# Kernel tuning notes

Measured on AMD Instinct MI355X. Metric: run time of the kernel, lower is better.

## Reference

```python
import jax, jax.numpy as jnp
import numpy as np

WINDOW_SYNC = 20   # min(20, T//2) with T=8192
WINDOW_SURGE = 10
BN_EPS = 1e-5      # BatchNorm1d eval-mode, running_mean=0, running_var=1


def _corr_matrix(x):
    # x: [w, A] observations x variables -> [A, A] Pearson correlation
    xc = x - x.mean(0)
    cov = xc.T @ xc
    d = jnp.sqrt(jnp.diag(cov))
    return cov / (d[:, None] * d[None, :])


def _offdiag_mean(C):
    A = C.shape[0]
    return (C.sum() - jnp.trace(C)) / (A * (A - 1))


def _rolling_offdiag_corr(returns, window):
    # mean off-diagonal correlation over each trailing window [i-window, i)
    T, A = returns.shape
    starts = jnp.arange(T - window)
    def one(s):
        w = jax.lax.dynamic_slice(returns, (s, 0), (window, A))
        return _offdiag_mean(_corr_matrix(w))
    return jax.vmap(one)(starts)


def setup_inputs() -> dict:
    key = jax.random.key(0)
    ks = jax.random.split(key, 10)
    T, A, H = 8192, 128, 128
    returns_sequence = jax.random.normal(ks[0], (T, A), dtype=jnp.float32) * 0.02
    positions = jax.random.normal(ks[1], (A,), dtype=jnp.float32)
    s1 = 1.0 / np.sqrt(2 * A)
    s2 = 1.0 / np.sqrt(H)
    s3 = 1.0 / np.sqrt(H // 2)
    return {
        "returns_sequence": returns_sequence,
        "positions": positions,
        "w1": jax.random.uniform(ks[2], (2 * A, H), jnp.float32, -s1, s1),
        "b1": jax.random.uniform(ks[3], (H,), jnp.float32, -s1, s1),
        "gamma": jnp.ones((H,), jnp.float32),
        "beta": jnp.zeros((H,), jnp.float32),
        "w2": jax.random.uniform(ks[4], (H, H // 2), jnp.float32, -s2, s2),
        "b2": jax.random.uniform(ks[5], (H // 2,), jnp.float32, -s2, s2),
        "w3": jax.random.uniform(ks[6], (H // 2, 3), jnp.float32, -s3, s3),
        "b3": jax.random.uniform(ks[7], (3,), jnp.float32, -s3, s3),
    }


def reference(returns_sequence, positions, w1, b1, gamma, beta, w2, b2, w3, b3):
    returns = returns_sequence
    T, A = returns.shape

    # ---- herding index ----
    cs_std = jnp.std(returns, axis=1, ddof=1)                 # [T]
    herding_trend = -jnp.diff(cs_std).mean()
    avg_dispersion = cs_std.mean()
    herding_index = jnp.clip(herding_trend / (avg_dispersion + 1e-6) + 0.5, 0.0, 1.0)

    # ---- synchronization ----
    corr = _corr_matrix(returns)                              # [A, A]
    avg_correlation = _offdiag_mean(corr)
    rolling = _rolling_offdiag_corr(returns, WINDOW_SYNC)     # [T-20]
    phase_locking = (rolling > 0.7).astype(jnp.float32).mean()
    eigvals = jnp.linalg.eigvalsh(corr)
    sync_indicator = eigvals.max() / A
    sync_risk = jnp.minimum(1.0, sync_indicator * avg_correlation)

    # ---- diversity loss ----
    return_diversity = 1.0 - jnp.abs(corr).mean()             # includes diagonal (as in torch)
    pa = jnp.abs(positions)
    position_diversity = 1.0 - (pa / pa.sum()).max()
    diversity_loss = 1.0 - jnp.sqrt(return_diversity * position_diversity)

    # ---- correlation surge ----
    rolling10 = _rolling_offdiag_corr(returns, WINDOW_SURGE)  # [T-10]
    recent = rolling10[-5:].mean()
    historical = rolling10[:-5].mean()
    surge_raw = jnp.clip((recent - historical) / historical, 0.0, 1.0)
    correlation_surge = jnp.where(historical > 0, surge_raw, 0.0)

    # ---- phase coupling (pairwise sign concordance) ----
    signs = jnp.sign(returns)                                 # [T, A]
    classes = jnp.array([-1.0, 0.0, 1.0], dtype=returns.dtype)
    I = (signs[None, :, :] == classes[:, None, None]).astype(returns.dtype)  # [3, T, A]
    M = jnp.einsum('cta,ctb->ab', I, I) / T                   # eq-fraction matrix [A, A]
    avg_concordance = _offdiag_mean(M)
    phase_coupling = jnp.clip((avg_concordance - 0.5) * 2.0, 0.0, 1.0)

    # ---- herding detector MLP (BatchNorm1d in eval mode) ----
    feats = jnp.concatenate([returns[-1], positions])         # [2A]
    h = jax.nn.relu(feats @ w1 + b1)
    h = gamma * (h / jnp.sqrt(1.0 + BN_EPS)) + beta
    h = jax.nn.relu(h @ w2 + b2)
    logits = h @ w3 + b3
    herding_severity = jax.nn.softmax(logits)[2]

    collective_risk = (herding_index + sync_risk + diversity_loss) / 3.0

    return jnp.stack([herding_index, herding_severity, sync_risk, phase_locking,
                      diversity_loss, correlation_surge, phase_coupling, collective_risk])
```

## Files before the change

### kernel.cpp

```cpp
#include <hip/hip_runtime.h>
#include <math.h>

#define TN 8192
#define AN 128
#define NW20 (TN - 20)
#define NW10 (TN - 10)

#define NB_GRAM 128
#define NB_ROW  512
#define NB_R20  511
#define NB_R10  512
#define NB_WORK (NB_GRAM + NB_ROW + NB_R20 + NB_R10)

#define WS_STD0 0
#define WS_STDL 1
#define WS_SPEC 8
#define WS_BLK  200
#define WS_DEND 4096

template <int W>
__device__ __forceinline__ void roll_strip4(const float* __restrict__ x,
                                            int s0, int nwin, int lane,
                                            double& accA, double& accB) {
  constexpr int NR = W + 3;
  float a0[NR], a1[NR];
#pragma unroll
  for (int t = 0; t < NR; ++t) {
    int r = s0 + t; r = (r < TN) ? r : (TN - 1);
    float2 v = *(const float2*)(x + (size_t)r * AN + 2 * lane);
    a0[t] = v.x; a1[t] = v.y;
  }
#pragma unroll
  for (int w4 = 0; w4 < 4; ++w4) {
    int s = s0 + w4;
    if (s < nwin) {
      float sf0 = 0.f, sf1 = 0.f;
#pragma unroll
      for (int t = 0; t < W; ++t) { sf0 += a0[w4 + t]; sf1 += a1[w4 + t]; }
      float mu0 = sf0 / W, mu1 = sf1 / W;
      float v0 = 0.f, v1 = 0.f;
#pragma unroll
      for (int t = 0; t < W; ++t) {
        float d0 = a0[w4 + t] - mu0, d1 = a1[w4 + t] - mu1;
        v0 += d0 * d0; v1 += d1 * d1;
      }
      float i0 = 1.0f / sqrtf(v0), i1 = 1.0f / sqrtf(v1);
      float q[W];
#pragma unroll
      for (int t = 0; t < W; ++t)
        q[t] = (a0[w4 + t] - mu0) * i0 + (a1[w4 + t] - mu1) * i1;
      int n = W;
#pragma unroll
      for (int o = 1; o <= 32; o <<= 1) {
#pragma unroll
        for (int k = 0; k < n; ++k) q[k] += __shfl_xor(q[k], o);
        if (n > 1) {
          int nh = n >> 1;
          bool hi = (lane & o) != 0;
#pragma unroll
          for (int k = 0; k < nh; ++k) q[k] = hi ? q[2 * k + 1] : q[2 * k];
          if (n & 1) { q[nh] = q[2 * nh]; n = nh + 1; } else { n = nh; }
        }
      }
      float alpha = (W == 20) ? ((lane & 16) ? 0.125f : 0.5f)
                              : ((lane & 8) ? 0.0625f : 0.25f);
      float r = q[0] * q[0] * alpha;
#pragma unroll
      for (int o = 32; o; o >>= 1) r += __shfl_xor(r, o);
      if (lane == 0) {
        double off = ((double)r - (double)AN) / ((double)AN * (AN - 1));
        if (W == 20) {
          accA += (off > 0.7) ? 1.0 : 0.0;
        } else {
          accA += off;
          if (s >= TN - W - 5) accB += off;
        }
      }
    }
  }
}

__global__ void __launch_bounds__(256) k_main(const float* __restrict__ x,
                                              double* __restrict__ wsd,
                                              float* __restrict__ pc,
                                              float* __restrict__ pdg,
                                              float* __restrict__ pg) {
  __shared__ union {
    float stage[8][AN];
    double tacc[4][2];
  } sm;
  const int b = blockIdx.x;
  const int tid = threadIdx.x;
  const int lane = tid & 63;
  const int w = tid >> 6;

  if (b < NB_GRAM) {
    int i0 = (tid >> 4) * 8;
    int j0 = (tid & 15) * 8;
    int lrow = tid >> 5;
    int lcol = (tid & 31) * 4;
    const float* xs = x + (size_t)b * 64 * AN;
    float acc[8][8];
#pragma unroll
    for (int a = 0; a < 8; ++a)
#pragma unroll
      for (int c = 0; c < 8; ++c) acc[a][c] = 0.f;
    float4 v = *(const float4*)(xs + lrow * AN + lcol);
    for (int it = 0; it < 8; ++it) {
      __syncthreads();
      *(float4*)(&sm.stage[lrow][lcol]) = v;
      __syncthreads();
      if (it + 1 < 8)
        v = *(const float4*)(xs + ((it + 1) * 8 + lrow) * AN + lcol);
#pragma unroll
      for (int r = 0; r < 8; ++r) {
        float aa[8], bb[8];
        *(float4*)(aa) = *(const float4*)(&sm.stage[r][i0]);
        *(float4*)(aa + 4) = *(const float4*)(&sm.stage[r][i0 + 4]);
        *(float4*)(bb) = *(const float4*)(&sm.stage[r][j0]);
        *(float4*)(bb + 4) = *(const float4*)(&sm.stage[r][j0 + 4]);
#pragma unroll
        for (int ai = 0; ai < 8; ++ai)
#pragma unroll
          for (int bj = 0; bj < 8; ++bj)
            acc[ai][bj] = fmaf(aa[ai], bb[bj], acc[ai][bj]);
      }
    }
    float* dst = pg + (size_t)b * (AN * AN);
#pragma unroll
    for (int ai = 0; ai < 8; ++ai)
#pragma unroll
      for (int bj = 0; bj < 8; bj += 4)
        *(float4*)(dst + (i0 + ai) * AN + j0 + bj) =
            make_float4(acc[ai][bj], acc[ai][bj + 1], acc[ai][bj + 2],
                        acc[ai][bj + 3]);
    if ((tid >> 4) == (tid & 15)) {
#pragma unroll
      for (int k = 0; k < 8; ++k) pdg[b * AN + i0 + k] = acc[k][k];
    }
    if (tid < AN) {
      float cs = 0.f;
      for (int r = 0; r < 64; ++r) cs += xs[r * AN + tid];
      pc[b * AN + tid] = cs;
    }
    return;
  }

  if (b < NB_GRAM + NB_ROW) {
    int rb = b - NB_GRAM;
    double sstd = 0.0, sconc = 0.0;
    for (int rr = 0; rr < 4; ++rr) {
      int t = rb * 16 + w * 4 + rr;
      float2 xv = *(const float2*)(x + (size_t)t * AN + 2 * lane);
      float x0 = xv.x, x1 = xv.y;
      float s = x0 + x1;
#pragma unroll
      for (int o = 32; o; o >>= 1) s += __shfl_xor(s, o);
      float mean = s * (1.0f / AN);
      float d0 = x0 - mean, d1 = x1 - mean;
      float q = d0 * d0 + d1 * d1;
#pragma unroll
      for (int o = 32; o; o >>= 1) q += __shfl_xor(q, o);
      float sd = sqrtf(q / (float)(AN - 1));
      int pk = (int)(x0 < 0.f) + (int)(x1 < 0.f)
             + (((int)(x0 == 0.f) + (int)(x1 == 0.f)) << 10)
             + (((int)(x0 > 0.f) + (int)(x1 > 0.f)) << 20);
#pragma unroll
      for (int o = 32; o; o >>= 1) pk += __shfl_xor(pk, o);
      if (lane == 0) {
        int nn = pk & 1023, nz = (pk >> 10) & 1023, np = (pk >> 20) & 1023;
        sconc += (double)nn * nn + (double)nz * nz + (double)np * np;
        sstd += (double)sd;
        if (t == 0) wsd[WS_STD0] = (double)sd;
        if (t == TN - 1) wsd[WS_STDL] = (double)sd;
      }
    }
    if (lane == 0) { sm.tacc[w][0] = sstd; sm.tacc[w][1] = sconc; }
    __syncthreads();
    if (tid == 0) {
      wsd[WS_BLK + (size_t)b * 2 + 0] =
          sm.tacc[0][0] + sm.tacc[1][0] + sm.tacc[2][0] + sm.tacc[3][0];
      wsd[WS_BLK + (size_t)b * 2 + 1] =
          sm.tacc[0][1] + sm.tacc[1][1] + sm.tacc[2][1] + sm.tacc[3][1];
    }
    return;
  }

  if (b < NB_GRAM + NB_ROW + NB_R20) {
    int s0 = (b - (NB_GRAM + NB_ROW)) * 16 + w * 4;
    double cnt = 0.0, dummy = 0.0;
    roll_strip4<20>(x, s0, NW20, lane, cnt, dummy);
    if (lane == 0) { sm.tacc[w][0] = cnt; }
    __syncthreads();
    if (tid == 0)
      wsd[WS_BLK + (size_t)b * 2 + 0] =
          sm.tacc[0][0] + sm.tacc[1][0] + sm.tacc[2][0] + sm.tacc[3][0];
    return;
  }

  {
    int s0 = (b - (NB_GRAM + NB_ROW + NB_R20)) * 16 + w * 4;
    double s10 = 0.0, s10l5 = 0.0;
    roll_strip4<10>(x, s0, NW10, lane, s10, s10l5);
    if (lane == 0) { sm.tacc[w][0] = s10; sm.tacc[w][1] = s10l5; }
    __syncthreads();
    if (tid == 0) {
      wsd[WS_BLK + (size_t)b * 2 + 0] =
          sm.tacc[0][0] + sm.tacc[1][0] + sm.tacc[2][0] + sm.tacc[3][0];
      wsd[WS_BLK + (size_t)b * 2 + 1] =
          sm.tacc[0][1] + sm.tacc[1][1] + sm.tacc[2][1] + sm.tacc[3][1];
    }
  }
}

__global__ void __launch_bounds__(256) k_fold(const float* __restrict__ pc,
                                              const float* __restrict__ pdg,
                                              const float* __restrict__ pg,
                                              double* __restrict__ wsd,
                                              float* __restrict__ corr) {
  __shared__ double r0[256], r1[256], r2[256], r3[256], r4[256];
  int b = blockIdx.x;
  int t = threadIdx.x;
  if (b < 64) {
    __shared__ double muS[AN], dS[AN];
    if (t < AN) {
      double cs = 0.0, dg = 0.0;
      for (int s = 0; s < NB_GRAM; ++s) {
        cs += (double)pc[s * AN + t];
        dg += (double)pdg[s * AN + t];
      }
      double mu = cs / (double)TN;
      muS[t] = mu;
      dS[t] = sqrt(dg - (double)TN * mu * mu);
    }
    __syncthreads();
    int e = b * 256 + t;
    int i = e >> 7, j = e & (AN - 1);
    double cv = 0.0;
    for (int s = 0; s < NB_GRAM; ++s) cv += (double)pg[(size_t)s * (AN * AN) + e];
    cv -= (double)TN * muS[i] * muS[j];
    double c = cv / (dS[i] * dS[j]);
    corr[e] = (float)c;
    r0[t] = c;
    r1[t] = fabs(c);
    r2[t] = (i == j) ? c : 0.0;
    __syncthreads();
    for (int sft = 128; sft; sft >>= 1) {
      if (t < sft) { r0[t] += r0[t + sft]; r1[t] += r1[t + sft]; r2[t] += r2[t + sft]; }
      __syncthreads();
    }
    if (t == 0) {
      wsd[WS_SPEC + b * 3 + 0] = r0[0];
      wsd[WS_SPEC + b * 3 + 1] = r1[0];
      wsd[WS_SPEC + b * 3 + 2] = r2[0];
    }
  } else {
    double a = 0.0, bc = 0.0, cnt = 0.0, s10 = 0.0, s10l5 = 0.0;
    for (int k = NB_GRAM + t; k < NB_WORK; k += 256) {
      const double* p = wsd + WS_BLK + (size_t)k * 2;
      if (k < NB_GRAM + NB_ROW) { a += p[0]; bc += p[1]; }
      else if (k < NB_GRAM + NB_ROW + NB_R20) cnt += p[0];
      else { s10 += p[0]; s10l5 += p[1]; }
    }
    r0[t] = a; r1[t] = bc; r2[t] = cnt; r3[t] = s10; r4[t] = s10l5;
    __syncthreads();
    for (int sft = 128; sft; sft >>= 1) {
      if (t < sft) {
        r0[t] += r0[t + sft]; r1[t] += r1[t + sft]; r2[t] += r2[t + sft];
        r3[t] += r3[t + sft]; r4[t] += r4[t + sft];
      }
      __syncthreads();
    }
    if (t == 0) {
      wsd[2] = r0[0];
      wsd[3] = r1[0];
      wsd[4] = r2[0];
      wsd[5] = r3[0];
      wsd[6] = r4[0];
    }
  }
}

__global__ void __launch_bounds__(256) k_spec_tail(
    const float* __restrict__ x, const float* __restrict__ pos,
    const float* __restrict__ w1, const float* __restrict__ b1,
    const float* __restrict__ gamma, const float* __restrict__ beta,
    const float* __restrict__ w2, const float* __restrict__ b2,
    const float* __restrict__ w3, const float* __restrict__ b3,
    const double* __restrict__ wsd, const float* __restrict__ corr,
    float* __restrict__ out) {
  __shared__ float vv[AN], prt[256], un[AN], red[4];
  __shared__ double spec[3];
  __shared__ float f[2 * AN], h1[AN], h2[64], lg[3];
  int t = threadIdx.x;
  int lane = t & 63;
  int w = t >> 6;
  if (t < 64) {
    double s0 = wsd[WS_SPEC + t * 3 + 0];
    double s1 = wsd[WS_SPEC + t * 3 + 1];
    double s2 = wsd[WS_SPEC + t * 3 + 2];
#pragma unroll
    for (int o = 32; o; o >>= 1) {
      s0 += __shfl_xor(s0, o);
      s1 += __shfl_xor(s1, o);
      s2 += __shfl_xor(s2, o);
    }
    if (t == 0) { spec[0] = s0; spec[1] = s1; spec[2] = s2; }
  }
  f[t] = (t < AN) ? x[(size_t)(TN - 1) * AN + t] : pos[t - AN];
  if (t < AN) vv[t] = 1.0f;
  __syncthreads();
  int ri = t & (AN - 1), hh = t >> 7;
  const float4* rp = (const float4*)(corr + ri * AN + hh * 64);
  float lam = 0.0f;
  for (int it = 0; it < 12; ++it) {
    const float4* vp = (const float4*)(&vv[hh * 64]);
    float acc = 0.f;
#pragma unroll
    for (int k = 0; k < 16; ++k) {
      float4 a = rp[k], bv = vp[k];
      acc += a.x * bv.x + a.y * bv.y + a.z * bv.z + a.w * bv.w;
    }
    prt[t] = acc;
    __syncthreads();
    if (t < AN) {
      float u = prt[t] + prt[t + 128];
      un[t] = u;
      float sq = u * u;
#pragma unroll
      for (int o = 32; o; o >>= 1) sq += __shfl_xor(sq, o);
      if (lane == 0) red[w] = sq;
    }
    __syncthreads();
    lam = sqrtf(red[0] + red[1]);
    if (t < AN) vv[t] = un[t] / lam;
    __syncthreads();
  }
  {
    int n = t & 127, h = t >> 7;
    float acc = 0.f;
    const float* wcol = w1 + h * 128 * AN + n;
    const float* fv = f + h * 128;
    for (int k = 0; k < 128; ++k) acc = fmaf(fv[k], wcol[k * AN], acc);
    prt[t] = acc;
  }
  __syncthreads();
  if (t < AN) {
    float acc = b1[t] + prt[t] + prt[t + 128];
    acc = fmaxf(acc, 0.0f);
    h1[t] = gamma[t] * (acc / sqrtf(1.0f + 1e-5f)) + beta[t];
  }
  __syncthreads();
  if (t < 64) {
    float acc = b2[t];
    for (int k = 0; k < AN; ++k) acc = fmaf(h1[k], w2[k * 64 + t], acc);
    h2[t] = fmaxf(acc, 0.0f);
  }
  __syncthreads();
  if (t < 3) {
    float acc = b3[t];
    for (int k = 0; k < 64; ++k) acc = fmaf(h2[k], w3[k * 3 + t], acc);
    lg[t] = acc;
  }
  __syncthreads();
  if (t != 0) return;
  float m = fmaxf(lg[0], fmaxf(lg[1], lg[2]));
  float e0 = expf(lg[0] - m), e1 = expf(lg[1] - m), e2 = expf(lg[2] - m);
  double sev = (double)(e2 / (e0 + e1 + e2));
  double sumstd = wsd[2], conc = wsd[3], cnt20 = wsd[4];
  double sum10 = wsd[5], sum10l5 = wsd[6];
  double avg_disp = sumstd / (double)TN;
  double trend = -(wsd[WS_STDL] - wsd[WS_STD0]) / (double)(TN - 1);
  double hi = trend / (avg_disp + 1e-6) + 0.5;
  hi = fmin(1.0, fmax(0.0, hi));
  double avg_corr = (spec[0] - spec[2]) / ((double)AN * (AN - 1));
  double sync_ind = (double)lam / (double)AN;
  double sync_risk = fmin(1.0, sync_ind * avg_corr);
  double pl = cnt20 / (double)(TN - 20);
  double rd = 1.0 - spec[1] / ((double)AN * AN);
  double pasum = 0.0, pamax = 0.0;
  for (int k = 0; k < AN; ++k) {
    double pa = fabs((double)pos[k]);
    pasum += pa;
    if (pa > pamax) pamax = pa;
  }
  double pd = 1.0 - pamax / pasum;
  double dl = 1.0 - sqrt(rd * pd);
  double recent = sum10l5 / 5.0;
  double hist = (sum10 - sum10l5) / (double)(TN - 10 - 5);
  double sraw = (recent - hist) / hist;
  sraw = fmin(1.0, fmax(0.0, sraw));
  double surge = (hist > 0.0) ? sraw : 0.0;
  double ac = (conc / (double)TN - (double)AN) / ((double)AN * (AN - 1));
  double pcup = fmin(1.0, fmax(0.0, (ac - 0.5) * 2.0));
  double cr = (hi + sync_risk + dl) / 3.0;
  out[0] = (float)hi;
  out[1] = (float)sev;
  out[2] = (float)sync_risk;
  out[3] = (float)pl;
  out[4] = (float)dl;
  out[5] = (float)surge;
  out[6] = (float)pcup;
  out[7] = (float)cr;
}

extern "C" void kernel_launch(void* const* d_in, const int* in_sizes, int n_in,
                              void* d_out, int out_size, void* d_ws, size_t ws_size,
                              hipStream_t stream) {
  const float* x     = (const float*)d_in[0];
  const float* pos   = (const float*)d_in[1];
  const float* w1    = (const float*)d_in[2];
  const float* b1    = (const float*)d_in[3];
  const float* gamma = (const float*)d_in[4];
  const float* beta  = (const float*)d_in[5];
  const float* w2    = (const float*)d_in[6];
  const float* b2    = (const float*)d_in[7];
  const float* w3    = (const float*)d_in[8];
  const float* b3    = (const float*)d_in[9];
  float* out = (float*)d_out;
  double* wsd = (double*)d_ws;
  float* corr = (float*)(wsd + WS_DEND);
  float* pc   = corr + AN * AN;
  float* pdg  = pc + NB_GRAM * AN;
  float* pg   = pdg + NB_GRAM * AN;

  k_main<<<NB_WORK, 256, 0, stream>>>(x, wsd, pc, pdg, pg);
  k_fold<<<65, 256, 0, stream>>>(pc, pdg, pg, wsd, corr);
  k_spec_tail<<<1, 256, 0, stream>>>(x, pos, w1, b1, gamma, beta, w2, b2,
                                     w3, b3, wsd, corr, out);
}
```

Measured before the change: 125.6 us.

## Fuse fold and tail kernels into one 1024-thread block with fewer Gram slices

```diff
diff --git a/kernel.cpp b/kernel.cpp
--- a/kernel.cpp
+++ b/kernel.cpp
@@ -6,16 +6,18 @@
 #define NW20 (TN - 20)
 #define NW10 (TN - 10)
 
-#define NB_GRAM 128
+#define NSL     32
 #define NB_ROW  512
 #define NB_R20  511
 #define NB_R10  512
-#define NB_WORK (NB_GRAM + NB_ROW + NB_R20 + NB_R10)
+#define RB0     NSL
+#define R20B0   (RB0 + NB_ROW)
+#define R10B0   (R20B0 + NB_R20)
+#define NB_WORK (R10B0 + NB_R10)
 
 #define WS_STD0 0
 #define WS_STDL 1
-#define WS_SPEC 8
-#define WS_BLK  200
+#define WS_BLK  8
 #define WS_DEND 4096
 
 template <int W>
@@ -94,23 +96,23 @@
   const int lane = tid & 63;
   const int w = tid >> 6;
 
-  if (b < NB_GRAM) {
+  if (b < NSL) {
     int i0 = (tid >> 4) * 8;
     int j0 = (tid & 15) * 8;
     int lrow = tid >> 5;
     int lcol = (tid & 31) * 4;
-    const float* xs = x + (size_t)b * 64 * AN;
+    const float* xs = x + (size_t)b * 256 * AN;
     float acc[8][8];
 #pragma unroll
     for (int a = 0; a < 8; ++a)
 #pragma unroll
       for (int c = 0; c < 8; ++c) acc[a][c] = 0.f;
     float4 v = *(const float4*)(xs + lrow * AN + lcol);
-    for (int it = 0; it < 8; ++it) {
+    for (int it = 0; it < 32; ++it) {
       __syncthreads();
       *(float4*)(&sm.stage[lrow][lcol]) = v;
       __syncthreads();
-      if (it + 1 < 8)
+      if (it + 1 < 32)
         v = *(const float4*)(xs + ((it + 1) * 8 + lrow) * AN + lcol);
 #pragma unroll
       for (int r = 0; r < 8; ++r) {
@@ -140,14 +142,14 @@
     }
     if (tid < AN) {
       float cs = 0.f;
-      for (int r = 0; r < 64; ++r) cs += xs[r * AN + tid];
+      for (int r = 0; r < 256; ++r) cs += xs[r * AN + tid];
       pc[b * AN + tid] = cs;
     }
     return;
   }
 
-  if (b < NB_GRAM + NB_ROW) {
-    int rb = b - NB_GRAM;
+  if (b < R20B0) {
+    int rb = b - RB0;
     double sstd = 0.0, sconc = 0.0;
     for (int rr = 0; rr < 4; ++rr) {
       int t = rb * 16 + w * 4 + rr;
@@ -186,8 +188,8 @@
     return;
   }
 
-  if (b < NB_GRAM + NB_ROW + NB_R20) {
-    int s0 = (b - (NB_GRAM + NB_ROW)) * 16 + w * 4;
+  if (b < R10B0) {
+    int s0 = (b - R20B0) * 16 + w * 4;
     double cnt = 0.0, dummy = 0.0;
     roll_strip4<20>(x, s0, NW20, lane, cnt, dummy);
     if (lane == 0) { sm.tacc[w][0] = cnt; }
@@ -199,7 +201,7 @@
   }
 
   {
-    int s0 = (b - (NB_GRAM + NB_ROW + NB_R20)) * 16 + w * 4;
+    int s0 = (b - R10B0) * 16 + w * 4;
     double s10 = 0.0, s10l5 = 0.0;
     roll_strip4<10>(x, s0, NW10, lane, s10, s10l5);
     if (lane == 0) { sm.tacc[w][0] = s10; sm.tacc[w][1] = s10l5; }
@@ -213,119 +215,102 @@
   }
 }
 
-__global__ void __launch_bounds__(256) k_fold(const float* __restrict__ pc,
-                                              const float* __restrict__ pdg,
-                                              const float* __restrict__ pg,
-                                              double* __restrict__ wsd,
-                                              float* __restrict__ corr) {
-  __shared__ double r0[256], r1[256], r2[256], r3[256], r4[256];
-  int b = blockIdx.x;
-  int t = threadIdx.x;
-  if (b < 64) {
-    __shared__ double muS[AN], dS[AN];
-    if (t < AN) {
-      double cs = 0.0, dg = 0.0;
-      for (int s = 0; s < NB_GRAM; ++s) {
-        cs += (double)pc[s * AN + t];
-        dg += (double)pdg[s * AN + t];
-      }
-      double mu = cs / (double)TN;
-      muS[t] = mu;
-      dS[t] = sqrt(dg - (double)TN * mu * mu);
-    }
-    __syncthreads();
-    int e = b * 256 + t;
-    int i = e >> 7, j = e & (AN - 1);
-    double cv = 0.0;
-    for (int s = 0; s < NB_GRAM; ++s) cv += (double)pg[(size_t)s * (AN * AN) + e];
-    cv -= (double)TN * muS[i] * muS[j];
-    double c = cv / (dS[i] * dS[j]);
-    corr[e] = (float)c;
-    r0[t] = c;
-    r1[t] = fabs(c);
-    r2[t] = (i == j) ? c : 0.0;
-    __syncthreads();
-    for (int sft = 128; sft; sft >>= 1) {
-      if (t < sft) { r0[t] += r0[t + sft]; r1[t] += r1[t + sft]; r2[t] += r2[t + sft]; }
-      __syncthreads();
-    }
-    if (t == 0) {
-      wsd[WS_SPEC + b * 3 + 0] = r0[0];
-      wsd[WS_SPEC + b * 3 + 1] = r1[0];
-      wsd[WS_SPEC + b * 3 + 2] = r2[0];
-    }
-  } else {
-    double a = 0.0, bc = 0.0, cnt = 0.0, s10 = 0.0, s10l5 = 0.0;
-    for (int k = NB_GRAM + t; k < NB_WORK; k += 256) {
-      const double* p = wsd + WS_BLK + (size_t)k * 2;
-      if (k < NB_GRAM + NB_ROW) { a += p[0]; bc += p[1]; }
-      else if (k < NB_GRAM + NB_ROW + NB_R20) cnt += p[0];
-      else { s10 += p[0]; s10l5 += p[1]; }
-    }
-    r0[t] = a; r1[t] = bc; r2[t] = cnt; r3[t] = s10; r4[t] = s10l5;
-    __syncthreads();
-    for (int sft = 128; sft; sft >>= 1) {
-      if (t < sft) {
-        r0[t] += r0[t + sft]; r1[t] += r1[t + sft]; r2[t] += r2[t + sft];
-        r3[t] += r3[t + sft]; r4[t] += r4[t + sft];
-      }
-      __syncthreads();
-    }
-    if (t == 0) {
-      wsd[2] = r0[0];
-      wsd[3] = r1[0];
-      wsd[4] = r2[0];
-      wsd[5] = r3[0];
-      wsd[6] = r4[0];
-    }
-  }
-}
-
-__global__ void __launch_bounds__(256) k_spec_tail(
+__global__ void __launch_bounds__(1024) k_tail(
     const float* __restrict__ x, const float* __restrict__ pos,
     const float* __restrict__ w1, const float* __restrict__ b1,
     const float* __restrict__ gamma, const float* __restrict__ beta,
     const float* __restrict__ w2, const float* __restrict__ b2,
     const float* __restrict__ w3, const float* __restrict__ b3,
-    const double* __restrict__ wsd, const float* __restrict__ corr,
+    const double* __restrict__ wsd, const float* __restrict__ pc,
+    const float* __restrict__ pdg, const float* __restrict__ pg,
     float* __restrict__ out) {
-  __shared__ float vv[AN], prt[256], un[AN], red[4];
-  __shared__ double spec[3];
+  __shared__ float cS[AN * 130];
+  __shared__ double muD[AN], dD[AN];
+  __shared__ double wred[16][8];
+  __shared__ double tiny[8];
+  __shared__ float vv[AN], prt[1024], un[AN], red[2];
   __shared__ float f[2 * AN], h1[AN], h2[64], lg[3];
-  int t = threadIdx.x;
-  int lane = t & 63;
-  int w = t >> 6;
-  if (t < 64) {
-    double s0 = wsd[WS_SPEC + t * 3 + 0];
-    double s1 = wsd[WS_SPEC + t * 3 + 1];
-    double s2 = wsd[WS_SPEC + t * 3 + 2];
-#pragma unroll
-    for (int o = 32; o; o >>= 1) {
-      s0 += __shfl_xor(s0, o);
-      s1 += __shfl_xor(s1, o);
-      s2 += __shfl_xor(s2, o);
-    }
-    if (t == 0) { spec[0] = s0; spec[1] = s1; spec[2] = s2; }
-  }
-  f[t] = (t < AN) ? x[(size_t)(TN - 1) * AN + t] : pos[t - AN];
-  if (t < AN) vv[t] = 1.0f;
-  __syncthreads();
-  int ri = t & (AN - 1), hh = t >> 7;
-  const float4* rp = (const float4*)(corr + ri * AN + hh * 64);
+  const int tid = threadIdx.x;
+  const int lane = tid & 63;
+  const int w = tid >> 6;
+
+  if (tid < 2 * AN)
+    f[tid] = (tid < AN) ? x[(size_t)(TN - 1) * AN + tid] : pos[tid - AN];
+  if (tid < AN) {
+    double cs = 0.0, dg = 0.0;
+    for (int s = 0; s < NSL; ++s) {
+      cs += (double)pc[s * AN + tid];
+      dg += (double)pdg[s * AN + tid];
+    }
+    double mu = cs / (double)TN;
+    muD[tid] = mu;
+    dD[tid] = sqrt(dg - (double)TN * mu * mu);
+  }
+  __syncthreads();
+  double c0 = 0.0, c1 = 0.0, c2 = 0.0;
+#pragma unroll
+  for (int g = 0; g < 4; ++g) {
+    int base = tid * 4 + g * 4096;
+    float4 s4 = make_float4(0.f, 0.f, 0.f, 0.f);
+    for (int s = 0; s < NSL; ++s) {
+      float4 v = *(const float4*)(pg + (size_t)s * (AN * AN) + base);
+      s4.x += v.x; s4.y += v.y; s4.z += v.z; s4.w += v.w;
+    }
+    int i = base >> 7, j = base & (AN - 1);
+    double mi = muD[i];
+    double cv[4] = {(double)s4.x, (double)s4.y, (double)s4.z, (double)s4.w};
+#pragma unroll
+    for (int k = 0; k < 4; ++k) {
+      double c = (cv[k] - (double)TN * mi * muD[j + k]) / (dD[i] * dD[j + k]);
+      cS[i * 130 + j + k] = (float)c;
+      c0 += c;
+      c1 += fabs(c);
+      if (i == (j + k)) c2 += c;
+    }
+  }
+  double v0 = 0, v1 = 0, v2 = 0, v3 = 0, v4 = 0;
+  for (int k = RB0 + tid; k < NB_WORK; k += 1024) {
+    const double* p = wsd + WS_BLK + (size_t)k * 2;
+    if (k < R20B0) { v0 += p[0]; v1 += p[1]; }
+    else if (k < R10B0) v2 += p[0];
+    else { v3 += p[0]; v4 += p[1]; }
+  }
+#pragma unroll
+  for (int o = 32; o; o >>= 1) {
+    v0 += __shfl_xor(v0, o); v1 += __shfl_xor(v1, o);
+    v2 += __shfl_xor(v2, o); v3 += __shfl_xor(v3, o);
+    v4 += __shfl_xor(v4, o);
+    c0 += __shfl_xor(c0, o); c1 += __shfl_xor(c1, o);
+    c2 += __shfl_xor(c2, o);
+  }
+  if (lane == 0) {
+    wred[w][0] = v0; wred[w][1] = v1; wred[w][2] = v2; wred[w][3] = v3;
+    wred[w][4] = v4; wred[w][5] = c0; wred[w][6] = c1; wred[w][7] = c2;
+  }
+  if (tid < AN) vv[tid] = 1.0f;
+  __syncthreads();
+  if (tid < 8) {
+    double s = 0.0;
+    for (int k = 0; k < 16; ++k) s += wred[k][tid];
+    tiny[tid] = s;
+  }
+  __syncthreads();
+  const int ri = tid & (AN - 1);
+  const int seg = tid >> 7;
+  const float* rowp = &cS[ri * 130 + seg * 16];
   float lam = 0.0f;
   for (int it = 0; it < 12; ++it) {
-    const float4* vp = (const float4*)(&vv[hh * 64]);
+    const float* vp = &vv[seg * 16];
     float acc = 0.f;
 #pragma unroll
-    for (int k = 0; k < 16; ++k) {
-      float4 a = rp[k], bv = vp[k];
-      acc += a.x * bv.x + a.y * bv.y + a.z * bv.z + a.w * bv.w;
-    }
-    prt[t] = acc;
-    __syncthreads();
-    if (t < AN) {
-      float u = prt[t] + prt[t + 128];
-      un[t] = u;
+    for (int k = 0; k < 16; ++k) acc += rowp[k] * vp[k];
+    prt[tid] = acc;
+    __syncthreads();
+    if (tid < AN) {
+      float u = 0.f;
+#pragma unroll
+      for (int s = 0; s < 8; ++s) u += prt[tid + 128 * s];
+      un[tid] = u;
       float sq = u * u;
 #pragma unroll
       for (int o = 32; o; o >>= 1) sq += __shfl_xor(sq, o);
@@ -333,51 +318,66 @@
     }
     __syncthreads();
     lam = sqrtf(red[0] + red[1]);
-    if (t < AN) vv[t] = un[t] / lam;
+    if (tid < AN) vv[tid] = un[tid] / lam;
     __syncthreads();
   }
   {
-    int n = t & 127, h = t >> 7;
+    int n = tid & 127, g = tid >> 7;
     float acc = 0.f;
-    const float* wcol = w1 + h * 128 * AN + n;
-    const float* fv = f + h * 128;
-    for (int k = 0; k < 128; ++k) acc = fmaf(fv[k], wcol[k * AN], acc);
-    prt[t] = acc;
-  }
-  __syncthreads();
-  if (t < AN) {
-    float acc = b1[t] + prt[t] + prt[t + 128];
+    const float* wcol = w1 + (g * 32) * AN + n;
+    const float* fv = f + g * 32;
+#pragma unroll
+    for (int k = 0; k < 32; ++k) acc = fmaf(fv[k], wcol[k * AN], acc);
+    prt[tid] = acc;
+  }
+  __syncthreads();
+  if (tid < AN) {
+    float acc = b1[tid];
+#pragma unroll
+    for (int s = 0; s < 8; ++s) acc += prt[tid + 128 * s];
     acc = fmaxf(acc, 0.0f);
-    h1[t] = gamma[t] * (acc / sqrtf(1.0f + 1e-5f)) + beta[t];
-  }
-  __syncthreads();
-  if (t < 64) {
-    float acc = b2[t];
-    for (int k = 0; k < AN; ++k) acc = fmaf(h1[k], w2[k * 64 + t], acc);
-    h2[t] = fmaxf(acc, 0.0f);
-  }
-  __syncthreads();
-  if (t < 3) {
-    float acc = b3[t];
-    for (int k = 0; k < 64; ++k) acc = fmaf(h2[k], w3[k * 3 + t], acc);
-    lg[t] = acc;
-  }
-  __syncthreads();
-  if (t != 0) return;
+    h1[tid] = gamma[tid] * (acc / sqrtf(1.0f + 1e-5f)) + beta[tid];
+  }
+  __syncthreads();
+  if (tid < 512) {
+    int n = tid & 63, g = tid >> 6;
+    float acc = 0.f;
+    const float* wcol = w2 + (g * 16) * 64 + n;
+    const float* hv = h1 + g * 16;
+#pragma unroll
+    for (int k = 0; k < 16; ++k) acc = fmaf(hv[k], wcol[k * 64], acc);
+    prt[tid] = acc;
+  }
+  __syncthreads();
+  if (tid < 64) {
+    float acc = b2[tid];
+#pragma unroll
+    for (int s = 0; s < 8; ++s) acc += prt[tid + 64 * s];
+    h2[tid] = fmaxf(acc, 0.0f);
+  }
+  __syncthreads();
+  if (tid < 3) {
+    float acc = b3[tid];
+    for (int k = 0; k < 64; ++k) acc = fmaf(h2[k], w3[k * 3 + tid], acc);
+    lg[tid] = acc;
+  }
+  __syncthreads();
+  if (tid != 0) return;
   float m = fmaxf(lg[0], fmaxf(lg[1], lg[2]));
   float e0 = expf(lg[0] - m), e1 = expf(lg[1] - m), e2 = expf(lg[2] - m);
   double sev = (double)(e2 / (e0 + e1 + e2));
-  double sumstd = wsd[2], conc = wsd[3], cnt20 = wsd[4];
-  double sum10 = wsd[5], sum10l5 = wsd[6];
+  double sumstd = tiny[0], conc = tiny[1], cnt20 = tiny[2];
+  double sum10 = tiny[3], sum10l5 = tiny[4];
+  double csum = tiny[5], cabs = tiny[6], ctrace = tiny[7];
   double avg_disp = sumstd / (double)TN;
   double trend = -(wsd[WS_STDL] - wsd[WS_STD0]) / (double)(TN - 1);
   double hi = trend / (avg_disp + 1e-6) + 0.5;
   hi = fmin(1.0, fmax(0.0, hi));
-  double avg_corr = (spec[0] - spec[2]) / ((double)AN * (AN - 1));
+  double avg_corr = (csum - ctrace) / ((double)AN * (AN - 1));
   double sync_ind = (double)lam / (double)AN;
   double sync_risk = fmin(1.0, sync_ind * avg_corr);
   double pl = cnt20 / (double)(TN - 20);
-  double rd = 1.0 - spec[1] / ((double)AN * AN);
+  double rd = 1.0 - cabs / ((double)AN * AN);
   double pasum = 0.0, pamax = 0.0;
   for (int k = 0; k < AN; ++k) {
     double pa = fabs((double)pos[k]);
@@ -419,13 +419,11 @@
   const float* b3    = (const float*)d_in[9];
   float* out = (float*)d_out;
   double* wsd = (double*)d_ws;
-  float* corr = (float*)(wsd + WS_DEND);
-  float* pc   = corr + AN * AN;
-  float* pdg  = pc + NB_GRAM * AN;
-  float* pg   = pdg + NB_GRAM * AN;
+  float* pc   = (float*)(wsd + WS_DEND);
+  float* pdg  = pc + NSL * AN;
+  float* pg   = pdg + NSL * AN;
 
   k_main<<<NB_WORK, 256, 0, stream>>>(x, wsd, pc, pdg, pg);
-  k_fold<<<65, 256, 0, stream>>>(pc, pdg, pg, wsd, corr);
-  k_spec_tail<<<1, 256, 0, stream>>>(x, pos, w1, b1, gamma, beta, w2, b2,
-                                     w3, b3, wsd, corr, out);
+  k_tail<<<1, 1024, 0, stream>>>(x, pos, w1, b1, gamma, beta, w2, b2, w3, b3,
+                                 wsd, pc, pdg, pg, out);
 }
```

After: 167.7 us. 1.33x slower.
